# Kernel tuning notes

Hardware: AMD Instinct MI355X
Metric: run time of the kernel (lower is better)

Reference implementation:

```python
import jax, jax.numpy as jnp
import numpy as np

USR_NUM = 100000
D_IN = 32
D_HID = 32
D_MID = 16
D_OUT = 2
N_EDGES = 1600000
EPS = 1e-16  # matches torch_geometric.utils.softmax denominator eps


def _glorot(key, shape):
    fan_in, fan_out = shape[0], shape[1]
    lim = np.sqrt(6.0 / (fan_in + fan_out))
    return jax.random.uniform(key, shape, jnp.float32, -lim, lim)


def setup_inputs() -> dict:
    key = jax.random.key(0)
    ks = jax.random.split(key, 16)
    inp = {
        "edge_index": jax.random.randint(ks[0], (2, N_EDGES), 0, USR_NUM, dtype=jnp.int64)
        if jax.config.jax_enable_x64 else jax.random.randint(ks[0], (2, N_EDGES), 0, USR_NUM).astype(jnp.int32),
        "emb": jax.random.normal(ks[1], (USR_NUM, D_IN), jnp.float32),
        # conv1: TransformerConv(32 -> 32, heads=1)
        "Wq1": _glorot(ks[2], (D_IN, D_HID)), "bq1": jnp.zeros((D_HID,), jnp.float32),
        "Wk1": _glorot(ks[3], (D_IN, D_HID)), "bk1": jnp.zeros((D_HID,), jnp.float32),
        "Wv1": _glorot(ks[4], (D_IN, D_HID)), "bv1": jnp.zeros((D_HID,), jnp.float32),
        "Ws1": _glorot(ks[5], (D_IN, D_HID)), "bs1": jnp.zeros((D_HID,), jnp.float32),
        # conv2: TransformerConv(32 -> 16, heads=1)
        "Wq2": _glorot(ks[6], (D_HID, D_MID)), "bq2": jnp.zeros((D_MID,), jnp.float32),
        "Wk2": _glorot(ks[7], (D_HID, D_MID)), "bk2": jnp.zeros((D_MID,), jnp.float32),
        "Wv2": _glorot(ks[8], (D_HID, D_MID)), "bv2": jnp.zeros((D_MID,), jnp.float32),
        "Ws2": _glorot(ks[9], (D_HID, D_MID)), "bs2": jnp.zeros((D_MID,), jnp.float32),
        # output: Linear(16 -> 2)
        "Wo": _glorot(ks[10], (D_MID, D_OUT)), "bo": jnp.zeros((D_OUT,), jnp.float32),
    }
    return inp


def transformer_conv(x, src, dst, Wq, bq, Wk, bk, Wv, bv, Ws, bs, n_nodes):
    # edge (j=src -> i=dst): alpha_ij = softmax_i( <q_i, k_j> / sqrt(d) )
    d = Wq.shape[1]
    q = (x @ Wq + bq)[dst]          # [E, d]
    k = (x @ Wk + bk)[src]          # [E, d]
    v = (x @ Wv + bv)[src]          # [E, d]
    alpha = jnp.sum(q * k, axis=-1) / jnp.sqrt(jnp.float32(d))  # [E]
    # segment softmax over incoming edges of each destination node
    seg_max = jax.ops.segment_max(alpha, dst, num_segments=n_nodes)  # [N]
    e = jnp.exp(alpha - seg_max[dst])
    seg_sum = jax.ops.segment_sum(e, dst, num_segments=n_nodes)      # [N]
    w = e / (seg_sum[dst] + EPS)
    agg = jax.ops.segment_sum(v * w[:, None], dst, num_segments=n_nodes)  # [N, d]
    return agg + x @ Ws + bs  # root/skip connection (PyG default root_weight=True)


def reference(edge_index, emb,
              Wq1, bq1, Wk1, bk1, Wv1, bv1, Ws1, bs1,
              Wq2, bq2, Wk2, bk2, Wv2, bv2, Ws2, bs2,
              Wo, bo):
    src, dst = edge_index[0], edge_index[1]
    h = transformer_conv(emb, src, dst, Wq1, bq1, Wk1, bk1, Wv1, bv1, Ws1, bs1, USR_NUM)
    h = jax.nn.relu(h)
    h = transformer_conv(h, src, dst, Wq2, bq2, Wk2, bk2, Wv2, bv2, Ws2, bs2, USR_NUM)
    h = jax.nn.relu(h)
    return h @ Wo + bo  # [N, 2]
```

## Files before the change

kernel.cpp:

```cpp
#include <hip/hip_runtime.h>
#include <hip/hip_bf16.h>

typedef __hip_bfloat16 bf16;
typedef unsigned int uint;
typedef unsigned short ushort;

#define N_NODES 100000
#define N_EDGES_C 1600000
#define NSB2 392
#define NSB2P 512
#define RND 2048
#define EPB (RND / 256)
#define NBIN 64
#define G_RAD ((N_EDGES_C + RND - 1) / RND)
#define HCAP 5632
#define NSLOT (NSB2 * 256)
#define NCHUNK 16
#define KEYN (256 * NCHUNK)

__device__ __forceinline__ float ldf(const void* p, long i, int isbf) {
    return isbf ? __bfloat162float(((const bf16*)p)[i]) : ((const float*)p)[i];
}
__device__ __forceinline__ int ldidx(const int* ei, long pos, int is64) {
    return is64 ? ei[2 * pos] : ei[pos];
}
__device__ __forceinline__ ushort bfb(float x) {
    bf16 h = __float2bfloat16(x);
    return *(ushort*)&h;
}
__device__ __forceinline__ float bl(uint u) { return __uint_as_float(u << 16); }
__device__ __forceinline__ float bh(uint u) { return __uint_as_float(u & 0xFFFF0000u); }

__global__ void setup_kernel(
    const void* emb, const int* ei,
    const void* Wq1, const void* bq1, const void* Wk1, const void* bk1,
    const void* Wv1, const void* bv1, const void* Ws1, const void* bs1,
    const void* Wq2, const void* bq2, const void* Wk2, const void* bk2,
    const void* Wv2, const void* bv2, const void* Ws2, const void* bs2,
    const void* Wo, const void* bo,
    int* flags, float* wp1, float* bp1, float* wp2, float* bp2, float* woF,
    int* curSB) {
    __shared__ int sf0;
    int t = threadIdx.x;
    if (t < 64) {
        const bf16* pb = (const bf16*)emb;
        int bad = 0;
        for (int i = t; i < 256; i += 64) {
            float v = __bfloat162float(pb[i]);
            if (!(v > -1.0e6f && v < 1.0e6f)) bad++;
        }
        int nz = 0;
        for (int i = 2 * t + 1; i < 256; i += 128) nz += (ei[i] != 0) ? 1 : 0;
#pragma unroll
        for (int m = 32; m >= 1; m >>= 1) {
            bad += __shfl_xor(bad, m, 64);
            nz  += __shfl_xor(nz, m, 64);
        }
        if (t == 0) {
            int f0 = (bad <= 8) ? 1 : 0;
            flags[0] = f0;
            flags[1] = (nz == 0) ? 1 : 0;
            sf0 = f0;
        }
    }
    __syncthreads();
    int isbf = sf0;
    for (int i = t; i < 1024; i += 256) {
        wp1[i]        = ldf(Wq1, i, isbf);
        wp1[1024 + i] = ldf(Wk1, i, isbf);
        wp1[2048 + i] = ldf(Wv1, i, isbf);
        wp1[3072 + i] = ldf(Ws1, i, isbf);
    }
    for (int i = t; i < 512; i += 256) {
        wp2[i]        = ldf(Wq2, i, isbf);
        wp2[512 + i]  = ldf(Wk2, i, isbf);
        wp2[1024 + i] = ldf(Wv2, i, isbf);
        wp2[1536 + i] = ldf(Ws2, i, isbf);
    }
    if (t < 32) {
        bp1[t] = ldf(bq1, t, isbf); bp1[32 + t] = ldf(bk1, t, isbf);
        bp1[64 + t] = ldf(bv1, t, isbf); bp1[96 + t] = ldf(bs1, t, isbf);
        woF[t] = ldf(Wo, t, isbf);
    }
    if (t < 16) {
        bp2[t] = ldf(bq2, t, isbf); bp2[16 + t] = ldf(bk2, t, isbf);
        bp2[32 + t] = ldf(bv2, t, isbf); bp2[48 + t] = ldf(bs2, t, isbf);
    }
    if (t < 2) woF[32 + t] = ldf(bo, t, isbf);
    curSB[t] = 0; curSB[t + 256] = 0;
}

template <int DOUT, bool RUNTIME_DTYPE>
__device__ __forceinline__ void node_linear_body(
    const void* __restrict__ X, const float* __restrict__ wpack,
    const float* __restrict__ bpack, const int* __restrict__ flags,
    float* __restrict__ q, ushort* __restrict__ kvb, float* __restrict__ s,
    int bid, float* __restrict__ sW, float* __restrict__ sbias, float* __restrict__ sX) {
    const int TPN = DOUT / 4;
    const int NPB = 256 / TPN;
    const int W_ELEMS = 4 * 32 * DOUT;

    const float4* wp4 = (const float4*)wpack;
    float4* sW4 = (float4*)sW;
    for (int i = threadIdx.x; i < W_ELEMS / 4; i += 256) sW4[i] = wp4[i];
    if (threadIdx.x < 4 * DOUT) sbias[threadIdx.x] = bpack[threadIdx.x];
    const int base = bid * NPB * 32;
    bool useBf = RUNTIME_DTYPE && (flags[0] != 0);
    if (useBf) {
        for (int i = threadIdx.x; i < NPB * 32; i += 256) {
            int g = base + i;
            float xv = (g < N_NODES * 32) ? __bfloat162float(((const bf16*)X)[g]) : 0.0f;
            sX[(i >> 5) * 36 + (i & 31)] = xv;
        }
    } else {
        for (int i = threadIdx.x; i < NPB * 32; i += 256) {
            int g = base + i;
            sX[(i >> 5) * 36 + (i & 31)] = (g < N_NODES * 32) ? ((const float*)X)[g] : 0.0f;
        }
    }
    __syncthreads();

    int l = threadIdx.x / TPN;
    int c4 = (threadIdx.x % TPN) * 4;
    int n = bid * NPB + l;
    if (n >= N_NODES) return;

    float xr[32];
#pragma unroll
    for (int j = 0; j < 8; j++) {
        float4 t4 = *(const float4*)&sX[l * 36 + 4 * j];
        xr[4 * j] = t4.x; xr[4 * j + 1] = t4.y; xr[4 * j + 2] = t4.z; xr[4 * j + 3] = t4.w;
    }
    float acc[4][4];
#pragma unroll
    for (int m = 0; m < 4; m++)
#pragma unroll
        for (int j = 0; j < 4; j++) acc[m][j] = sbias[m * DOUT + c4 + j];

#pragma unroll
    for (int t = 0; t < 32; t++) {
#pragma unroll
        for (int m = 0; m < 4; m++) {
            float4 w = *(const float4*)&sW[(m * 32 + t) * DOUT + c4];
            acc[m][0] += xr[t] * w.x;
            acc[m][1] += xr[t] * w.y;
            acc[m][2] += xr[t] * w.z;
            acc[m][3] += xr[t] * w.w;
        }
    }
    size_t o = (size_t)n * DOUT + c4;
    *(float4*)&q[o] = make_float4(acc[0][0], acc[0][1], acc[0][2], acc[0][3]);
    *(float4*)&s[o] = make_float4(acc[3][0], acc[3][1], acc[3][2], acc[3][3]);
    size_t okv = (size_t)n * 2 * DOUT + c4;
    ushort4 kp = make_ushort4(bfb(acc[1][0]), bfb(acc[1][1]), bfb(acc[1][2]), bfb(acc[1][3]));
    ushort4 vp = make_ushort4(bfb(acc[2][0]), bfb(acc[2][1]), bfb(acc[2][2]), bfb(acc[2][3]));
    *(ushort4*)&kvb[okv]        = kp;
    *(ushort4*)&kvb[okv + DOUT] = vp;
}

struct RadixS {
    int cnt[NSB2P]; int excl[NSB2P]; int gbase[NSB2P]; int wsum[4];
    uint sVal[RND]; ushort sSb[RND];
};
struct LinS { float sW[4096]; float sbias[128]; float sX[32 * 36]; };
union alignas(16) FusedS { RadixS r; LinS l; };

__global__ void __launch_bounds__(256, 4) fused_ra_nl(
    const int* __restrict__ ei, const int* __restrict__ flags,
    int* __restrict__ curSB, uint* __restrict__ pairsSB,
    const void* __restrict__ X, const float* __restrict__ wpack,
    const float* __restrict__ bpack,
    float* __restrict__ q, ushort* __restrict__ kvb, float* __restrict__ s) {
    __shared__ FusedS u;
    if (blockIdx.x >= G_RAD) {
        node_linear_body<32, true>(X, wpack, bpack, flags, q, kvb, s,
                                   (int)blockIdx.x - G_RAD, u.l.sW, u.l.sbias, u.l.sX);
        return;
    }
    int* cnt = u.r.cnt; int* excl = u.r.excl; int* gbase = u.r.gbase;
    uint* sVal = u.r.sVal; ushort* sSb = u.r.sSb;
    const int is64 = flags[1];
    int t = threadIdx.x;
    cnt[t] = 0; cnt[t + 256] = 0;
    __syncthreads();
    long base = (long)blockIdx.x * RND;

    int mySb[EPB]; int myRank[EPB]; uint myPk[EPB];
#pragma unroll
    for (int r = 0; r < EPB; r++) {
        long e = base + r * 256 + t;
        mySb[r] = -1;
        if (e < N_EDGES_C) {
            int d = ldidx(ei, (long)N_EDGES_C + e, is64);
            int src = ldidx(ei, e, is64);
            int sb = d >> 8;
            myPk[r] = (uint)src | ((uint)(d & 255) << 17);
            myRank[r] = atomicAdd(&cnt[sb], 1);
            mySb[r] = sb;
        }
    }
    __syncthreads();
    int v0 = cnt[2 * t], v1 = cnt[2 * t + 1];
    int sum2 = v0 + v1;
    int lane6 = t & 63, wid6 = t >> 6;
    int x = sum2;
#pragma unroll
    for (int off = 1; off < 64; off <<= 1) {
        int u2 = __shfl_up(x, off, 64);
        if (lane6 >= off) x += u2;
    }
    if (lane6 == 63) u.r.wsum[wid6] = x;
    __syncthreads();
    int wbase = 0;
#pragma unroll
    for (int w = 0; w < 4; w++) if (w < wid6) wbase += u.r.wsum[w];
    int basex = wbase + x - sum2;
    excl[2 * t]     = basex;
    excl[2 * t + 1] = basex + v0;
    __syncthreads();
#pragma unroll
    for (int r = 0; r < EPB; r++) {
        if (mySb[r] >= 0) {
            int pos = excl[mySb[r]] + myRank[r];
            sVal[pos] = myPk[r];
            sSb[pos] = (ushort)mySb[r];
        }
    }
    for (int i = t; i < NSB2P; i += 256)
        gbase[i] = (cnt[i] > 0) ? atomicAdd(&curSB[i], cnt[i]) : 0;
    __syncthreads();
    int tot = excl[NSB2P - 1] + cnt[NSB2P - 1];
    for (int i = t; i < tot; i += 256) {
        int sb = sSb[i];
        int gp = gbase[sb] + (i - excl[sb]);
        if (gp < HCAP)
            pairsSB[(size_t)sb * HCAP + gp] = sVal[i];
    }
}

__global__ void __launch_bounds__(256, 2) radix_b(
    const int* __restrict__ curSB, const uint* __restrict__ pairsSB,
    int* __restrict__ esrc,
    int* __restrict__ rowbeg, int* __restrict__ rowend,
    int* __restrict__ perm) {
    __shared__ uint sP[HCAP];
    __shared__ int dcnt[KEYN];
    __shared__ int dexcl[KEYN];
    __shared__ int dcur[KEYN];
    __shared__ int wsum[4];
    __shared__ int hbin[NBIN], hbase[NBIN], hcur[NBIN];
    int sbh = blockIdx.x;
    int t = threadIdx.x;
    int n = min(curSB[sbh], HCAP);
    for (int i = t; i < KEYN; i += 256) { dcnt[i] = 0; dcur[i] = 0; }
    if (t < NBIN) { hbin[t] = 0; hcur[t] = 0; }
    perm[sbh * 256 + t] = -1;
    __syncthreads();
    const uint* srcp = pairsSB + (size_t)sbh * HCAP;
    for (int i = t; i < n; i += 256) {
        uint pk = srcp[i];
        sP[i] = pk;
        int key = (int)((pk >> 17) & 255) * NCHUNK + (int)((pk & 0x1FFFFu) >> 13);
        atomicAdd(&dcnt[key], 1);
    }
    __syncthreads();
    const int kb = t * NCHUNK;
    int sum = 0;
#pragma unroll
    for (int j = 0; j < NCHUNK; j++) sum += dcnt[kb + j];
    int v = sum;
    int lane6 = t & 63, wid6 = t >> 6;
    int x = v;
#pragma unroll
    for (int off = 1; off < 64; off <<= 1) {
        int u2 = __shfl_up(x, off, 64);
        if (lane6 >= off) x += u2;
    }
    if (lane6 == 63) wsum[wid6] = x;
    __syncthreads();
    int wbase = 0;
#pragma unroll
    for (int w = 0; w < 4; w++) if (w < wid6) wbase += wsum[w];
    int myExcl = wbase + x - v;
    int run = myExcl;
#pragma unroll
    for (int j = 0; j < NCHUNK; j++) { dexcl[kb + j] = run; run += dcnt[kb + j]; }
    __syncthreads();
    const int EB = sbh * HCAP;
    int dst = sbh * 256 + t;
    int mybin = -1;
    if (dst < N_NODES) {
        rowbeg[dst] = EB + min(myExcl, HCAP);
        rowend[dst] = EB + min(myExcl + v, HCAP);
        mybin = min(v, NBIN - 1);
        atomicAdd(&hbin[mybin], 1);
    }
    __syncthreads();
    if (t < 64) {
        int hv = hbin[t];
        int sfx = hv;
#pragma unroll
        for (int off = 1; off < 64; off <<= 1) {
            int u2 = __shfl_down(sfx, off, 64);
            if (t + off < 64) sfx += u2;
        }
        hbase[t] = sfx - hv;
    }
    __syncthreads();
    if (dst < N_NODES) {
        int r = atomicAdd(&hcur[mybin], 1);
        perm[sbh * 256 + hbase[mybin] + r] = dst;
    }
    for (int i = t; i < n; i += 256) {
        uint pk = sP[i];
        int key = (int)((pk >> 17) & 255) * NCHUNK + (int)((pk & 0x1FFFFu) >> 13);
        int p2 = dexcl[key] + atomicAdd(&dcur[key], 1);
        if (p2 < HCAP) esrc[EB + p2] = (int)(pk & 0x1FFFF);
    }
}

template <int D, bool LAYER2>
__global__ void gather_attn(const int* __restrict__ perm,
                            const int* __restrict__ rowbeg, const int* __restrict__ rowend,
                            const int* __restrict__ esrc,
                            const float* __restrict__ q, const ushort* __restrict__ kvb,
                            const float* __restrict__ s,
                            const float* __restrict__ wp2,
                            const float* __restrict__ bp2,
                            const float* __restrict__ woF,
                            const int* __restrict__ flags,
                            float* __restrict__ q2o, ushort* __restrict__ kvb2o,
                            float* __restrict__ s2o,
                            void* __restrict__ out) {
    const int LPD = D / 8;
    const int LG  = 2 * LPD;
    const int G   = 64 / LG;
    __shared__ float sW2[LAYER2 ? 4 : 2048];
    __shared__ float sb2[LAYER2 ? 4 : 64];
    __shared__ float sH[LAYER2 ? 4 : 32 * 36];
    __shared__ int sDst[LAYER2 ? 4 : 32];

    if constexpr (!LAYER2) {
        for (int i = threadIdx.x; i < 2048; i += 256) sW2[i] = wp2[i];
        if (threadIdx.x < 64) sb2[threadIdx.x] = bp2[threadIdx.x];
    }

    int lane = threadIdx.x & 63;
    int W = (blockIdx.x * blockDim.x + threadIdx.x) >> 6;
    int g = lane / LG;
    int sub = lane % LG;
    int c = sub % LPD;
    int eh = sub / LPD;
    int idx = W * G + g;
    int dst = perm[idx];
    if constexpr (LAYER2) {
        if (dst < 0) return;
    }
    bool alive = (dst >= 0);

    const float rsq = (D == 32) ? 0.17677669529663689f : 0.25f;
    float4 qa = make_float4(0.f, 0.f, 0.f, 0.f), qb = qa;
    int beg = 0, end = 0;
    if (alive) {
        qa = *(const float4*)(q + (size_t)dst * D + 8 * c);
        qb = *(const float4*)(q + (size_t)dst * D + 8 * c + 4);
        beg = rowbeg[dst]; end = rowend[dst];
    }

    const char* kvbase = (const char*)kvb;
    const int ROW = 4 * D;
    const int koff = 16 * c;
    const int voff = 2 * D + 16 * c;

    float sum0 = 0.f, sum1 = 0.f;
    float a0[8] = {0,0,0,0,0,0,0,0};
    float a1[8] = {0,0,0,0,0,0,0,0};

    int ebase = beg + eh;
    uint4 kq[4], vq[4];
#pragma unroll
    for (int r = 0; r < 4; r++) {
        int pos = ebase + 2 * r;
        int sn = (pos < end) ? esrc[pos] : 0;
        const char* p = kvbase + (size_t)sn * ROW;
        kq[r] = *(const uint4*)(p + koff);
        vq[r] = *(const uint4*)(p + voff);
    }

    for (int e = ebase; e < end; e += 8) {
        uint4 kc[4], vc[4];
#pragma unroll
        for (int r = 0; r < 4; r++) { kc[r] = kq[r]; vc[r] = vq[r]; }
#pragma unroll
        for (int r = 0; r < 4; r++) {
            int pos = e + 8 + 2 * r;
            if (pos < end) {
                const char* p = kvbase + (size_t)esrc[pos] * ROW;
                kq[r] = *(const uint4*)(p + koff);
                vq[r] = *(const uint4*)(p + voff);
            }
        }
#pragma unroll
        for (int r = 0; r < 4; r++) {
            if (e + 2 * r < end) {
                uint4 kA = kc[r], vA = vc[r];
                float pd = qa.x * bl(kA.x) + qa.y * bh(kA.x) + qa.z * bl(kA.y) + qa.w * bh(kA.y)
                         + qb.x * bl(kA.z) + qb.y * bh(kA.z) + qb.z * bl(kA.w) + qb.w * bh(kA.w);
#pragma unroll
                for (int m = LPD / 2; m >= 1; m >>= 1) pd += __shfl_xor(pd, m, LPD);
                float ex = __expf(fminf(fmaxf(pd * rsq, -80.0f), 80.0f));
                if (r & 1) {
                    sum1 += ex;
                    a1[0] += bl(vA.x) * ex; a1[1] += bh(vA.x) * ex;
                    a1[2] += bl(vA.y) * ex; a1[3] += bh(vA.y) * ex;
                    a1[4] += bl(vA.z) * ex; a1[5] += bh(vA.z) * ex;
                    a1[6] += bl(vA.w) * ex; a1[7] += bh(vA.w) * ex;
                } else {
                    sum0 += ex;
                    a0[0] += bl(vA.x) * ex; a0[1] += bh(vA.x) * ex;
                    a0[2] += bl(vA.y) * ex; a0[3] += bh(vA.y) * ex;
                    a0[4] += bl(vA.z) * ex; a0[5] += bh(vA.z) * ex;
                    a0[6] += bl(vA.w) * ex; a0[7] += bh(vA.w) * ex;
                }
            }
        }
    }
    float sT = sum0 + sum1;
    sT += __shfl_xor(sT, LPD, LG);
    float aT[8];
#pragma unroll
    for (int j = 0; j < 8; j++) {
        aT[j] = a0[j] + a1[j];
        aT[j] += __shfl_xor(aT[j], LPD, LG);
    }
    float inv = 1.0f / (sT + 1e-16f);
    float4 sa = make_float4(0.f, 0.f, 0.f, 0.f), sbv = sa;
    if (alive) {
        sa  = *(const float4*)(s + (size_t)dst * D + 8 * c);
        sbv = *(const float4*)(s + (size_t)dst * D + 8 * c + 4);
    }
    float h[8];
    h[0] = aT[0] * inv + sa.x;  h[1] = aT[1] * inv + sa.y;
    h[2] = aT[2] * inv + sa.z;  h[3] = aT[3] * inv + sa.w;
    h[4] = aT[4] * inv + sbv.x; h[5] = aT[5] * inv + sbv.y;
    h[6] = aT[6] * inv + sbv.z; h[7] = aT[7] * inv + sbv.w;
#pragma unroll
    for (int j = 0; j < 8; j++) h[j] = h[j] > 0.0f ? h[j] : 0.0f;

    if constexpr (!LAYER2) {
        int gl = (threadIdx.x >> 6) * G + g;
        if (alive && eh == 0) {
            *(float4*)&sH[gl * 36 + 8 * c]     = make_float4(h[0], h[1], h[2], h[3]);
            *(float4*)&sH[gl * 36 + 8 * c + 4] = make_float4(h[4], h[5], h[6], h[7]);
        }
        if (c == 0 && eh == 0) sDst[gl] = dst;
        __syncthreads();
        if (threadIdx.x < 128) {
            int l = threadIdx.x >> 2;
            int c4 = (threadIdx.x & 3) * 4;
            int nd = sDst[l];
            if (nd >= 0) {
                float acc2[4][4];
#pragma unroll
                for (int m = 0; m < 4; m++)
#pragma unroll
                    for (int j = 0; j < 4; j++) acc2[m][j] = sb2[m * 16 + c4 + j];
#pragma unroll
                for (int t2 = 0; t2 < 32; t2++) {
                    float xv = sH[l * 36 + t2];
#pragma unroll
                    for (int m = 0; m < 4; m++) {
                        float4 w = *(const float4*)&sW2[(m * 32 + t2) * 16 + c4];
                        acc2[m][0] += xv * w.x;
                        acc2[m][1] += xv * w.y;
                        acc2[m][2] += xv * w.z;
                        acc2[m][3] += xv * w.w;
                    }
                }
                size_t o = (size_t)nd * 16 + c4;
                *(float4*)&q2o[o] = make_float4(acc2[0][0], acc2[0][1], acc2[0][2], acc2[0][3]);
                *(float4*)&s2o[o] = make_float4(acc2[3][0], acc2[3][1], acc2[3][2], acc2[3][3]);
                size_t okv = (size_t)nd * 32 + c4;
                ushort4 kp = make_ushort4(bfb(acc2[1][0]), bfb(acc2[1][1]), bfb(acc2[1][2]), bfb(acc2[1][3]));
                ushort4 vp = make_ushort4(bfb(acc2[2][0]), bfb(acc2[2][1]), bfb(acc2[2][2]), bfb(acc2[2][3]));
                *(ushort4*)&kvb2o[okv]      = kp;
                *(ushort4*)&kvb2o[okv + 16] = vp;
            }
        }
    } else {
        float p0 = 0.f, p1 = 0.f;
#pragma unroll
        for (int j = 0; j < 8; j++) {
            p0 += h[j] * woF[(8 * c + j) * 2 + 0];
            p1 += h[j] * woF[(8 * c + j) * 2 + 1];
        }
#pragma unroll
        for (int m = LPD / 2; m >= 1; m >>= 1) {
            p0 += __shfl_xor(p0, m, LPD);
            p1 += __shfl_xor(p1, m, LPD);
        }
        if (c == 0 && eh == 0) {
            float o0 = p0 + woF[32];
            float o1 = p1 + woF[33];
            if (flags[0]) {
                ((bf16*)out)[dst * 2 + 0] = __float2bfloat16(o0);
                ((bf16*)out)[dst * 2 + 1] = __float2bfloat16(o1);
            } else {
                ((float*)out)[dst * 2 + 0] = o0;
                ((float*)out)[dst * 2 + 1] = o1;
            }
        }
    }
}

extern "C" void kernel_launch(void* const* d_in, const int* in_sizes, int n_in,
                              void* d_out, int out_size, void* d_ws, size_t ws_size,
                              hipStream_t stream) {
    const int* ei  = (const int*)d_in[0];
    const void* emb = d_in[1];
    const void *Wq1 = d_in[2],  *bq1 = d_in[3];
    const void *Wk1 = d_in[4],  *bk1 = d_in[5];
    const void *Wv1 = d_in[6],  *bv1 = d_in[7];
    const void *Ws1 = d_in[8],  *bs1 = d_in[9];
    const void *Wq2 = d_in[10], *bq2 = d_in[11];
    const void *Wk2 = d_in[12], *bk2 = d_in[13];
    const void *Wv2 = d_in[14], *bv2 = d_in[15];
    const void *Ws2 = d_in[16], *bs2 = d_in[17];
    const void *Wo  = d_in[18], *bo  = d_in[19];

    const size_t ND   = (size_t)N_NODES * 32;
    const size_t ND16 = (size_t)N_NODES * 16;
    const size_t SBTOT = (size_t)NSB2 * HCAP;
    float* base   = (float*)d_ws;
    int*   flags  = (int*)base;
    float* wp1    = base + 64;
    float* bp1    = wp1 + 4096;
    float* wp2    = bp1 + 128;
    float* bp2    = wp2 + 2048;
    float* woF    = bp2 + 64;
    int*   curSB  = (int*)(woF + 64);
    int*   rowbeg = curSB + 512;
    int*   rowend = rowbeg + N_NODES;
    int*   perm   = rowend + N_NODES;
    float* p      = (float*)(perm + NSLOT);
    float* q      = p; p += ND;
    float* s      = p; p += ND;
    ushort* kvb   = (ushort*)p; p += ND;
    float* q2     = p; p += ND16;
    float* s2     = p; p += ND16;
    ushort* kvb2  = (ushort*)p; p += ND16;
    int*   esrc   = (int*)p; p += SBTOT;
    uint*  pairsSB = (uint*)p;

    const int B = 256;
    const int gNL32  = (N_NODES + 31) / 32;
    const int gFused = G_RAD + gNL32;
    const int gG1    = NSLOT / 8 / 4;
    const int gG2    = NSLOT / 16 / 4;

    setup_kernel<<<1, B, 0, stream>>>(emb, ei,
        Wq1, bq1, Wk1, bk1, Wv1, bv1, Ws1, bs1,
        Wq2, bq2, Wk2, bk2, Wv2, bv2, Ws2, bs2, Wo, bo,
        flags, wp1, bp1, wp2, bp2, woF, curSB);

    fused_ra_nl<<<gFused, B, 0, stream>>>(ei, flags, curSB, pairsSB,
                                          emb, wp1, bp1, q, kvb, s);

    radix_b<<<NSB2, B, 0, stream>>>(curSB, pairsSB, esrc, rowbeg, rowend, perm);

    gather_attn<32, false><<<gG1, B, 0, stream>>>(
        perm, rowbeg, rowend, esrc, q, kvb, s, wp2, bp2, nullptr, flags,
        q2, kvb2, s2, nullptr);

    gather_attn<16, true><<<gG2, B, 0, stream>>>(
        perm, rowbeg, rowend, esrc, q2, kvb2, s2, nullptr, nullptr, woF, flags,
        nullptr, nullptr, nullptr, d_out);
}
```

Measured before the change: 261.3 us.

## Split gather lanes into key and value halves with prefetched edge indices

Reworks the per-destination attention gather so half of each lane group loads the key chunk and the other half loads the value chunk of the same edge. Previously each lane loaded both key and value for alternating edges. Each edge row is now read contiguously across the group, and source indices are prefetched one stage ahead of the row loads. This cuts accumulator registers and the final cross-half reduction, but each lane now walks every edge, which doubles the per-lane exp and shuffle work. The workspace feature buffers are also aligned to 128 bytes.

```diff
diff --git a/kernel.cpp b/kernel.cpp
--- a/kernel.cpp
+++ b/kernel.cpp
@@ -332,9 +332,9 @@
                             float* __restrict__ q2o, ushort* __restrict__ kvb2o,
                             float* __restrict__ s2o,
                             void* __restrict__ out) {
-    const int LPD = D / 8;
-    const int LG  = 2 * LPD;
-    const int G   = 64 / LG;
+    const int LG = D / 4;
+    const int KL = LG / 2;
+    const int G  = 64 / LG;
     __shared__ float sW2[LAYER2 ? 4 : 2048];
     __shared__ float sb2[LAYER2 ? 4 : 64];
     __shared__ float sH[LAYER2 ? 4 : 32 * 36];
@@ -349,8 +349,8 @@
     int W = (blockIdx.x * blockDim.x + threadIdx.x) >> 6;
     int g = lane / LG;
     int sub = lane % LG;
-    int c = sub % LPD;
-    int eh = sub / LPD;
+    bool isK = (sub < KL);
+    int cv = sub - KL;
     int idx = W * G + g;
     int dst = perm[idx];
     if constexpr (LAYER2) {
@@ -359,101 +359,93 @@
     bool alive = (dst >= 0);
 
     const float rsq = (D == 32) ? 0.17677669529663689f : 0.25f;
-    float4 qa = make_float4(0.f, 0.f, 0.f, 0.f), qb = qa;
+    float qacc[8] = {0,0,0,0,0,0,0,0};
     int beg = 0, end = 0;
     if (alive) {
-        qa = *(const float4*)(q + (size_t)dst * D + 8 * c);
-        qb = *(const float4*)(q + (size_t)dst * D + 8 * c + 4);
+        if (isK) {
+            float4 qa = *(const float4*)(q + (size_t)dst * D + 8 * sub);
+            float4 qb = *(const float4*)(q + (size_t)dst * D + 8 * sub + 4);
+            qacc[0] = qa.x; qacc[1] = qa.y; qacc[2] = qa.z; qacc[3] = qa.w;
+            qacc[4] = qb.x; qacc[5] = qb.y; qacc[6] = qb.z; qacc[7] = qb.w;
+        }
         beg = rowbeg[dst]; end = rowend[dst];
     }
 
-    const char* kvbase = (const char*)kvb;
+    const char* kvbase = (const char*)kvb + 16 * sub;
     const int ROW = 4 * D;
-    const int koff = 16 * c;
-    const int voff = 2 * D + 16 * c;
-
-    float sum0 = 0.f, sum1 = 0.f;
-    float a0[8] = {0,0,0,0,0,0,0,0};
-    float a1[8] = {0,0,0,0,0,0,0,0};
-
-    int ebase = beg + eh;
-    uint4 kq[4], vq[4];
+
+    float sum = 0.f;
+
+    uint4 rv[4];
+    int sn1[4];
 #pragma unroll
     for (int r = 0; r < 4; r++) {
-        int pos = ebase + 2 * r;
-        int sn = (pos < end) ? esrc[pos] : 0;
-        const char* p = kvbase + (size_t)sn * ROW;
-        kq[r] = *(const uint4*)(p + koff);
-        vq[r] = *(const uint4*)(p + voff);
-    }
-
-    for (int e = ebase; e < end; e += 8) {
-        uint4 kc[4], vc[4];
-#pragma unroll
-        for (int r = 0; r < 4; r++) { kc[r] = kq[r]; vc[r] = vq[r]; }
+        int sn = (beg + r < end) ? esrc[beg + r] : 0;
+        rv[r] = *(const uint4*)(kvbase + (size_t)sn * ROW);
+    }
+#pragma unroll
+    for (int r = 0; r < 4; r++)
+        sn1[r] = (beg + 4 + r < end) ? esrc[beg + 4 + r] : 0;
+
+    for (int e = beg; e < end; e += 4) {
+        uint4 rc[4];
+#pragma unroll
+        for (int r = 0; r < 4; r++) rc[r] = rv[r];
 #pragma unroll
         for (int r = 0; r < 4; r++) {
-            int pos = e + 8 + 2 * r;
-            if (pos < end) {
-                const char* p = kvbase + (size_t)esrc[pos] * ROW;
-                kq[r] = *(const uint4*)(p + koff);
-                vq[r] = *(const uint4*)(p + voff);
-            }
+            if (e + 4 + r < end)
+                rv[r] = *(const uint4*)(kvbase + (size_t)sn1[r] * ROW);
         }
 #pragma unroll
         for (int r = 0; r < 4; r++) {
-            if (e + 2 * r < end) {
-                uint4 kA = kc[r], vA = vc[r];
-                float pd = qa.x * bl(kA.x) + qa.y * bh(kA.x) + qa.z * bl(kA.y) + qa.w * bh(kA.y)
-                         + qb.x * bl(kA.z) + qb.y * bh(kA.z) + qb.z * bl(kA.w) + qb.w * bh(kA.w);
-#pragma unroll
-                for (int m = LPD / 2; m >= 1; m >>= 1) pd += __shfl_xor(pd, m, LPD);
-                float ex = __expf(fminf(fmaxf(pd * rsq, -80.0f), 80.0f));
-                if (r & 1) {
-                    sum1 += ex;
-                    a1[0] += bl(vA.x) * ex; a1[1] += bh(vA.x) * ex;
-                    a1[2] += bl(vA.y) * ex; a1[3] += bh(vA.y) * ex;
-                    a1[4] += bl(vA.z) * ex; a1[5] += bh(vA.z) * ex;
-                    a1[6] += bl(vA.w) * ex; a1[7] += bh(vA.w) * ex;
-                } else {
-                    sum0 += ex;
-                    a0[0] += bl(vA.x) * ex; a0[1] += bh(vA.x) * ex;
-                    a0[2] += bl(vA.y) * ex; a0[3] += bh(vA.y) * ex;
-                    a0[4] += bl(vA.z) * ex; a0[5] += bh(vA.z) * ex;
-                    a0[6] += bl(vA.w) * ex; a0[7] += bh(vA.w) * ex;
+            if (e + 8 + r < end) sn1[r] = esrc[e + 8 + r];
+        }
+#pragma unroll
+        for (int r = 0; r < 4; r++) {
+            if (e + r < end) {
+                uint4 rA = rc[r];
+                float pd = 0.f;
+                if (isK) {
+                    pd = qacc[0] * bl(rA.x) + qacc[1] * bh(rA.x)
+                       + qacc[2] * bl(rA.y) + qacc[3] * bh(rA.y)
+                       + qacc[4] * bl(rA.z) + qacc[5] * bh(rA.z)
+                       + qacc[6] * bl(rA.w) + qacc[7] * bh(rA.w);
+                }
+#pragma unroll
+                for (int m = KL / 2; m >= 1; m >>= 1) pd += __shfl_xor(pd, m, KL);
+                float pdx = __shfl_xor(pd, KL, LG);
+                float pdf = isK ? pd : pdx;
+                float ex = __expf(fminf(fmaxf(pdf * rsq, -80.0f), 80.0f));
+                sum += ex;
+                if (!isK) {
+                    qacc[0] += bl(rA.x) * ex; qacc[1] += bh(rA.x) * ex;
+                    qacc[2] += bl(rA.y) * ex; qacc[3] += bh(rA.y) * ex;
+                    qacc[4] += bl(rA.z) * ex; qacc[5] += bh(rA.z) * ex;
+                    qacc[6] += bl(rA.w) * ex; qacc[7] += bh(rA.w) * ex;
                 }
             }
         }
     }
-    float sT = sum0 + sum1;
-    sT += __shfl_xor(sT, LPD, LG);
-    float aT[8];
-#pragma unroll
-    for (int j = 0; j < 8; j++) {
-        aT[j] = a0[j] + a1[j];
-        aT[j] += __shfl_xor(aT[j], LPD, LG);
-    }
-    float inv = 1.0f / (sT + 1e-16f);
-    float4 sa = make_float4(0.f, 0.f, 0.f, 0.f), sbv = sa;
-    if (alive) {
-        sa  = *(const float4*)(s + (size_t)dst * D + 8 * c);
-        sbv = *(const float4*)(s + (size_t)dst * D + 8 * c + 4);
-    }
+    float inv = 1.0f / (sum + 1e-16f);
     float h[8];
-    h[0] = aT[0] * inv + sa.x;  h[1] = aT[1] * inv + sa.y;
-    h[2] = aT[2] * inv + sa.z;  h[3] = aT[3] * inv + sa.w;
-    h[4] = aT[4] * inv + sbv.x; h[5] = aT[5] * inv + sbv.y;
-    h[6] = aT[6] * inv + sbv.z; h[7] = aT[7] * inv + sbv.w;
-#pragma unroll
-    for (int j = 0; j < 8; j++) h[j] = h[j] > 0.0f ? h[j] : 0.0f;
+    if (alive && !isK) {
+        float4 sa  = *(const float4*)(s + (size_t)dst * D + 8 * cv);
+        float4 sbv = *(const float4*)(s + (size_t)dst * D + 8 * cv + 4);
+        h[0] = qacc[0] * inv + sa.x;  h[1] = qacc[1] * inv + sa.y;
+        h[2] = qacc[2] * inv + sa.z;  h[3] = qacc[3] * inv + sa.w;
+        h[4] = qacc[4] * inv + sbv.x; h[5] = qacc[5] * inv + sbv.y;
+        h[6] = qacc[6] * inv + sbv.z; h[7] = qacc[7] * inv + sbv.w;
+#pragma unroll
+        for (int j = 0; j < 8; j++) h[j] = h[j] > 0.0f ? h[j] : 0.0f;
+    }
 
     if constexpr (!LAYER2) {
         int gl = (threadIdx.x >> 6) * G + g;
-        if (alive && eh == 0) {
-            *(float4*)&sH[gl * 36 + 8 * c]     = make_float4(h[0], h[1], h[2], h[3]);
-            *(float4*)&sH[gl * 36 + 8 * c + 4] = make_float4(h[4], h[5], h[6], h[7]);
-        }
-        if (c == 0 && eh == 0) sDst[gl] = dst;
+        if (alive && !isK) {
+            *(float4*)&sH[gl * 36 + 8 * cv]     = make_float4(h[0], h[1], h[2], h[3]);
+            *(float4*)&sH[gl * 36 + 8 * cv + 4] = make_float4(h[4], h[5], h[6], h[7]);
+        }
+        if (sub == 0) sDst[gl] = dst;
         __syncthreads();
         if (threadIdx.x < 128) {
             int l = threadIdx.x >> 2;
@@ -489,17 +481,16 @@
         }
     } else {
         float p0 = 0.f, p1 = 0.f;
-#pragma unroll
-        for (int j = 0; j < 8; j++) {
-            p0 += h[j] * woF[(8 * c + j) * 2 + 0];
-            p1 += h[j] * woF[(8 * c + j) * 2 + 1];
-        }
-#pragma unroll
-        for (int m = LPD / 2; m >= 1; m >>= 1) {
-            p0 += __shfl_xor(p0, m, LPD);
-            p1 += __shfl_xor(p1, m, LPD);
-        }
-        if (c == 0 && eh == 0) {
+        if (!isK) {
+#pragma unroll
+            for (int j = 0; j < 8; j++) {
+                p0 += h[j] * woF[(8 * cv + j) * 2 + 0];
+                p1 += h[j] * woF[(8 * cv + j) * 2 + 1];
+            }
+        }
+        p0 += __shfl_xor(p0, 1, 2);
+        p1 += __shfl_xor(p1, 1, 2);
+        if (sub == KL) {
             float o0 = p0 + woF[32];
             float o1 = p1 + woF[33];
             if (flags[0]) {
@@ -543,6 +534,7 @@
     int*   rowend = rowbeg + N_NODES;
     int*   perm   = rowend + N_NODES;
     float* p      = (float*)(perm + NSLOT);
+    p = (float*)(((uintptr_t)p + 127) & ~(uintptr_t)127);
     float* q      = p; p += ND;
     float* s      = p; p += ND;
     ushort* kvb   = (ushort*)p; p += ND;
```

Result: slower. 269.5 us (+3.1%).

## Drop edge-split lanes in gather, widen radix_b to 512 threads

Applied to the files above, without the earlier changes.

The gather kernels now give each destination node a single lane group of D/8 lanes that walks all of its edges, instead of two groups that each take half the edges and then combine with shuffles. This packs twice as many nodes per wave and removes the cross-half reduction, but each lane group now handles more serial edge iterations. The local radix sort runs 512 threads per block with half as many chunk keys, and uses atomics on the exclusive offsets in place of a separate cursor array. The workspace pointer is also aligned to 128 bytes.

```diff
diff --git a/kernel.cpp b/kernel.cpp
--- a/kernel.cpp
+++ b/kernel.cpp
@@ -15,7 +15,7 @@
 #define G_RAD ((N_EDGES_C + RND - 1) / RND)
 #define HCAP 5632
 #define NSLOT (NSB2 * 256)
-#define NCHUNK 16
+#define NCHUNK 8
 #define KEYN (256 * NCHUNK)
 
 __device__ __forceinline__ float ldf(const void* p, long i, int isbf) {
@@ -238,7 +238,7 @@
     }
 }
 
-__global__ void __launch_bounds__(256, 2) radix_b(
+__global__ void __launch_bounds__(512, 2) radix_b(
     const int* __restrict__ curSB, const uint* __restrict__ pairsSB,
     int* __restrict__ esrc,
     int* __restrict__ rowbeg, int* __restrict__ rowend,
@@ -246,50 +246,57 @@
     __shared__ uint sP[HCAP];
     __shared__ int dcnt[KEYN];
     __shared__ int dexcl[KEYN];
-    __shared__ int dcur[KEYN];
     __shared__ int wsum[4];
     __shared__ int hbin[NBIN], hbase[NBIN], hcur[NBIN];
     int sbh = blockIdx.x;
     int t = threadIdx.x;
     int n = min(curSB[sbh], HCAP);
-    for (int i = t; i < KEYN; i += 256) { dcnt[i] = 0; dcur[i] = 0; }
+    for (int i = t; i < KEYN; i += 512) dcnt[i] = 0;
     if (t < NBIN) { hbin[t] = 0; hcur[t] = 0; }
-    perm[sbh * 256 + t] = -1;
+    if (t < 256) perm[sbh * 256 + t] = -1;
     __syncthreads();
     const uint* srcp = pairsSB + (size_t)sbh * HCAP;
-    for (int i = t; i < n; i += 256) {
+    for (int i = t; i < n; i += 512) {
         uint pk = srcp[i];
         sP[i] = pk;
-        int key = (int)((pk >> 17) & 255) * NCHUNK + (int)((pk & 0x1FFFFu) >> 13);
+        int key = (int)((pk >> 17) & 255) * NCHUNK + (int)((pk & 0x1FFFFu) >> 14);
         atomicAdd(&dcnt[key], 1);
     }
     __syncthreads();
-    const int kb = t * NCHUNK;
-    int sum = 0;
-#pragma unroll
-    for (int j = 0; j < NCHUNK; j++) sum += dcnt[kb + j];
-    int v = sum;
-    int lane6 = t & 63, wid6 = t >> 6;
-    int x = v;
-#pragma unroll
-    for (int off = 1; off < 64; off <<= 1) {
-        int u2 = __shfl_up(x, off, 64);
-        if (lane6 >= off) x += u2;
-    }
-    if (lane6 == 63) wsum[wid6] = x;
-    __syncthreads();
-    int wbase = 0;
-#pragma unroll
-    for (int w = 0; w < 4; w++) if (w < wid6) wbase += wsum[w];
-    int myExcl = wbase + x - v;
-    int run = myExcl;
-#pragma unroll
-    for (int j = 0; j < NCHUNK; j++) { dexcl[kb + j] = run; run += dcnt[kb + j]; }
+    int v = 0, myExcl = 0;
+    if (t < 256) {
+        const int kb = t * NCHUNK;
+        int sum = 0;
+#pragma unroll
+        for (int j = 0; j < NCHUNK; j++) sum += dcnt[kb + j];
+        v = sum;
+        int lane6 = t & 63, wid6 = t >> 6;
+        int x = v;
+#pragma unroll
+        for (int off = 1; off < 64; off <<= 1) {
+            int u2 = __shfl_up(x, off, 64);
+            if (lane6 >= off) x += u2;
+        }
+        if (lane6 == 63) wsum[wid6] = x;
+        myExcl = x - v;
+    }
+    __syncthreads();
+    if (t < 256) {
+        int wid6 = t >> 6;
+        int wbase = 0;
+#pragma unroll
+        for (int w = 0; w < 4; w++) if (w < wid6) wbase += wsum[w];
+        myExcl += wbase;
+        const int kb = t * NCHUNK;
+        int run = myExcl;
+#pragma unroll
+        for (int j = 0; j < NCHUNK; j++) { dexcl[kb + j] = run; run += dcnt[kb + j]; }
+    }
     __syncthreads();
     const int EB = sbh * HCAP;
     int dst = sbh * 256 + t;
     int mybin = -1;
-    if (dst < N_NODES) {
+    if (t < 256 && dst < N_NODES) {
         rowbeg[dst] = EB + min(myExcl, HCAP);
         rowend[dst] = EB + min(myExcl + v, HCAP);
         mybin = min(v, NBIN - 1);
@@ -307,14 +314,14 @@
         hbase[t] = sfx - hv;
     }
     __syncthreads();
-    if (dst < N_NODES) {
+    if (t < 256 && dst < N_NODES) {
         int r = atomicAdd(&hcur[mybin], 1);
         perm[sbh * 256 + hbase[mybin] + r] = dst;
     }
-    for (int i = t; i < n; i += 256) {
+    for (int i = t; i < n; i += 512) {
         uint pk = sP[i];
-        int key = (int)((pk >> 17) & 255) * NCHUNK + (int)((pk & 0x1FFFFu) >> 13);
-        int p2 = dexcl[key] + atomicAdd(&dcur[key], 1);
+        int key = (int)((pk >> 17) & 255) * NCHUNK + (int)((pk & 0x1FFFFu) >> 14);
+        int p2 = atomicAdd(&dexcl[key], 1);
         if (p2 < HCAP) esrc[EB + p2] = (int)(pk & 0x1FFFF);
     }
 }
@@ -333,12 +340,11 @@
                             float* __restrict__ s2o,
                             void* __restrict__ out) {
     const int LPD = D / 8;
-    const int LG  = 2 * LPD;
-    const int G   = 64 / LG;
+    const int G = 64 / LPD;
     __shared__ float sW2[LAYER2 ? 4 : 2048];
     __shared__ float sb2[LAYER2 ? 4 : 64];
-    __shared__ float sH[LAYER2 ? 4 : 32 * 36];
-    __shared__ int sDst[LAYER2 ? 4 : 32];
+    __shared__ float sH[LAYER2 ? 4 : 64 * 36];
+    __shared__ int sDst[LAYER2 ? 4 : 64];
 
     if constexpr (!LAYER2) {
         for (int i = threadIdx.x; i < 2048; i += 256) sW2[i] = wp2[i];
@@ -346,12 +352,10 @@
     }
 
     int lane = threadIdx.x & 63;
-    int W = (blockIdx.x * blockDim.x + threadIdx.x) >> 6;
-    int g = lane / LG;
-    int sub = lane % LG;
-    int c = sub % LPD;
-    int eh = sub / LPD;
-    int idx = W * G + g;
+    int wave = (blockIdx.x * blockDim.x + threadIdx.x) >> 6;
+    int g = lane / LPD;
+    int c = lane % LPD;
+    int idx = wave * G + g;
     int dst = perm[idx];
     if constexpr (LAYER2) {
         if (dst < 0) return;
@@ -376,33 +380,30 @@
     float a0[8] = {0,0,0,0,0,0,0,0};
     float a1[8] = {0,0,0,0,0,0,0,0};
 
-    int ebase = beg + eh;
     uint4 kq[4], vq[4];
 #pragma unroll
     for (int r = 0; r < 4; r++) {
-        int pos = ebase + 2 * r;
-        int sn = (pos < end) ? esrc[pos] : 0;
+        int sn = (beg + r < end) ? esrc[beg + r] : 0;
         const char* p = kvbase + (size_t)sn * ROW;
         kq[r] = *(const uint4*)(p + koff);
         vq[r] = *(const uint4*)(p + voff);
     }
 
-    for (int e = ebase; e < end; e += 8) {
+    for (int e = beg; e < end; e += 4) {
         uint4 kc[4], vc[4];
 #pragma unroll
         for (int r = 0; r < 4; r++) { kc[r] = kq[r]; vc[r] = vq[r]; }
 #pragma unroll
         for (int r = 0; r < 4; r++) {
-            int pos = e + 8 + 2 * r;
-            if (pos < end) {
-                const char* p = kvbase + (size_t)esrc[pos] * ROW;
+            if (e + 4 + r < end) {
+                const char* p = kvbase + (size_t)esrc[e + 4 + r] * ROW;
                 kq[r] = *(const uint4*)(p + koff);
                 vq[r] = *(const uint4*)(p + voff);
             }
         }
 #pragma unroll
         for (int r = 0; r < 4; r++) {
-            if (e + 2 * r < end) {
+            if (e + r < end) {
                 uint4 kA = kc[r], vA = vc[r];
                 float pd = qa.x * bl(kA.x) + qa.y * bh(kA.x) + qa.z * bl(kA.y) + qa.w * bh(kA.y)
                          + qb.x * bl(kA.z) + qb.y * bh(kA.z) + qb.z * bl(kA.w) + qb.w * bh(kA.w);
@@ -425,67 +426,57 @@
             }
         }
     }
-    float sT = sum0 + sum1;
-    sT += __shfl_xor(sT, LPD, LG);
-    float aT[8];
-#pragma unroll
-    for (int j = 0; j < 8; j++) {
-        aT[j] = a0[j] + a1[j];
-        aT[j] += __shfl_xor(aT[j], LPD, LG);
-    }
-    float inv = 1.0f / (sT + 1e-16f);
+    float inv = 1.0f / (sum0 + sum1 + 1e-16f);
     float4 sa = make_float4(0.f, 0.f, 0.f, 0.f), sbv = sa;
     if (alive) {
         sa  = *(const float4*)(s + (size_t)dst * D + 8 * c);
         sbv = *(const float4*)(s + (size_t)dst * D + 8 * c + 4);
     }
     float h[8];
-    h[0] = aT[0] * inv + sa.x;  h[1] = aT[1] * inv + sa.y;
-    h[2] = aT[2] * inv + sa.z;  h[3] = aT[3] * inv + sa.w;
-    h[4] = aT[4] * inv + sbv.x; h[5] = aT[5] * inv + sbv.y;
-    h[6] = aT[6] * inv + sbv.z; h[7] = aT[7] * inv + sbv.w;
+    h[0] = (a0[0] + a1[0]) * inv + sa.x;  h[1] = (a0[1] + a1[1]) * inv + sa.y;
+    h[2] = (a0[2] + a1[2]) * inv + sa.z;  h[3] = (a0[3] + a1[3]) * inv + sa.w;
+    h[4] = (a0[4] + a1[4]) * inv + sbv.x; h[5] = (a0[5] + a1[5]) * inv + sbv.y;
+    h[6] = (a0[6] + a1[6]) * inv + sbv.z; h[7] = (a0[7] + a1[7]) * inv + sbv.w;
 #pragma unroll
     for (int j = 0; j < 8; j++) h[j] = h[j] > 0.0f ? h[j] : 0.0f;
 
     if constexpr (!LAYER2) {
         int gl = (threadIdx.x >> 6) * G + g;
-        if (alive && eh == 0) {
+        if (alive) {
             *(float4*)&sH[gl * 36 + 8 * c]     = make_float4(h[0], h[1], h[2], h[3]);
             *(float4*)&sH[gl * 36 + 8 * c + 4] = make_float4(h[4], h[5], h[6], h[7]);
         }
-        if (c == 0 && eh == 0) sDst[gl] = dst;
+        if (c == 0) sDst[gl] = dst;
         __syncthreads();
-        if (threadIdx.x < 128) {
-            int l = threadIdx.x >> 2;
-            int c4 = (threadIdx.x & 3) * 4;
-            int nd = sDst[l];
-            if (nd >= 0) {
-                float acc2[4][4];
-#pragma unroll
-                for (int m = 0; m < 4; m++)
-#pragma unroll
-                    for (int j = 0; j < 4; j++) acc2[m][j] = sb2[m * 16 + c4 + j];
-#pragma unroll
-                for (int t2 = 0; t2 < 32; t2++) {
-                    float xv = sH[l * 36 + t2];
-#pragma unroll
-                    for (int m = 0; m < 4; m++) {
-                        float4 w = *(const float4*)&sW2[(m * 32 + t2) * 16 + c4];
-                        acc2[m][0] += xv * w.x;
-                        acc2[m][1] += xv * w.y;
-                        acc2[m][2] += xv * w.z;
-                        acc2[m][3] += xv * w.w;
-                    }
+        int l = threadIdx.x >> 2;
+        int c4 = (threadIdx.x & 3) * 4;
+        int nd = sDst[l];
+        if (nd >= 0) {
+            float acc2[4][4];
+#pragma unroll
+            for (int m = 0; m < 4; m++)
+#pragma unroll
+                for (int j = 0; j < 4; j++) acc2[m][j] = sb2[m * 16 + c4 + j];
+#pragma unroll
+            for (int t2 = 0; t2 < 32; t2++) {
+                float xv = sH[l * 36 + t2];
+#pragma unroll
+                for (int m = 0; m < 4; m++) {
+                    float4 w = *(const float4*)&sW2[(m * 32 + t2) * 16 + c4];
+                    acc2[m][0] += xv * w.x;
+                    acc2[m][1] += xv * w.y;
+                    acc2[m][2] += xv * w.z;
+                    acc2[m][3] += xv * w.w;
                 }
-                size_t o = (size_t)nd * 16 + c4;
-                *(float4*)&q2o[o] = make_float4(acc2[0][0], acc2[0][1], acc2[0][2], acc2[0][3]);
-                *(float4*)&s2o[o] = make_float4(acc2[3][0], acc2[3][1], acc2[3][2], acc2[3][3]);
-                size_t okv = (size_t)nd * 32 + c4;
-                ushort4 kp = make_ushort4(bfb(acc2[1][0]), bfb(acc2[1][1]), bfb(acc2[1][2]), bfb(acc2[1][3]));
-                ushort4 vp = make_ushort4(bfb(acc2[2][0]), bfb(acc2[2][1]), bfb(acc2[2][2]), bfb(acc2[2][3]));
-                *(ushort4*)&kvb2o[okv]      = kp;
-                *(ushort4*)&kvb2o[okv + 16] = vp;
             }
+            size_t o = (size_t)nd * 16 + c4;
+            *(float4*)&q2o[o] = make_float4(acc2[0][0], acc2[0][1], acc2[0][2], acc2[0][3]);
+            *(float4*)&s2o[o] = make_float4(acc2[3][0], acc2[3][1], acc2[3][2], acc2[3][3]);
+            size_t okv = (size_t)nd * 32 + c4;
+            ushort4 kp = make_ushort4(bfb(acc2[1][0]), bfb(acc2[1][1]), bfb(acc2[1][2]), bfb(acc2[1][3]));
+            ushort4 vp = make_ushort4(bfb(acc2[2][0]), bfb(acc2[2][1]), bfb(acc2[2][2]), bfb(acc2[2][3]));
+            *(ushort4*)&kvb2o[okv]      = kp;
+            *(ushort4*)&kvb2o[okv + 16] = vp;
         }
     } else {
         float p0 = 0.f, p1 = 0.f;
@@ -499,7 +490,7 @@
             p0 += __shfl_xor(p0, m, LPD);
             p1 += __shfl_xor(p1, m, LPD);
         }
-        if (c == 0 && eh == 0) {
+        if (c == 0) {
             float o0 = p0 + woF[32];
             float o1 = p1 + woF[33];
             if (flags[0]) {
@@ -543,6 +534,7 @@
     int*   rowend = rowbeg + N_NODES;
     int*   perm   = rowend + N_NODES;
     float* p      = (float*)(perm + NSLOT);
+    p = (float*)(((uintptr_t)p + 127) & ~(uintptr_t)127);
     float* q      = p; p += ND;
     float* s      = p; p += ND;
     ushort* kvb   = (ushort*)p; p += ND;
@@ -555,8 +547,8 @@
     const int B = 256;
     const int gNL32  = (N_NODES + 31) / 32;
     const int gFused = G_RAD + gNL32;
-    const int gG1    = NSLOT / 8 / 4;
-    const int gG2    = NSLOT / 16 / 4;
+    const int gG1    = NSLOT / 64;
+    const int gG2    = NSLOT / 128;
 
     setup_kernel<<<1, B, 0, stream>>>(emb, ei,
         Wq1, bq1, Wk1, bk1, Wv1, bv1, Ws1, bs1,
@@ -566,7 +558,7 @@
     fused_ra_nl<<<gFused, B, 0, stream>>>(ei, flags, curSB, pairsSB,
                                           emb, wp1, bp1, q, kvb, s);
 
-    radix_b<<<NSB2, B, 0, stream>>>(curSB, pairsSB, esrc, rowbeg, rowend, perm);
+    radix_b<<<NSB2, 512, 0, stream>>>(curSB, pairsSB, esrc, rowbeg, rowend, perm);
 
     gather_attn<32, false><<<gG1, B, 0, stream>>>(
         perm, rowbeg, rowend, esrc, q, kvb, s, wp2, bp2, nullptr, flags,
```

Measured after the change: 259.3 us. No clear change (-0.8%).
